# Kernel tuning notes

Hardware: AMD Instinct MI355X
Metric: run time of the kernel (lower is better)

The kernel has to match this reference:

```python
import jax, jax.numpy as jnp
import numpy as np

B = 16
N = [4096, 1024, 256, 64, 16]
NF = [1, 16, 32, 64, 128, 256]
DEG = 6
KS = 5
LAT = 32


def spline_conv(x, edge_index, pseudo, W, root, bias):
    """SplineConv: open B-spline, degree 1, dim 3, kernel_size 5, sum aggregation (norm=False).
    x: [Nn, Cin], edge_index: [2, E] (src, dst), pseudo: [E, 3] in [0,1], W: [125, Cin, Cout]."""
    src, dst = edge_index[0], edge_index[1]
    v = pseudo * (KS - 1)                       # degree-1 open spline interval
    lo = jnp.clip(jnp.floor(v), 0.0, KS - 2)
    frac = v - lo                               # [E, 3]
    lo = lo.astype(jnp.int32)
    xs = x[src]                                 # [E, Cin] gather
    strides = jnp.array([1, KS, KS * KS], dtype=jnp.int32)
    msg = jnp.zeros((src.shape[0], W.shape[2]), dtype=x.dtype)
    for s in range(8):                          # (degree+1)^dim = 8 basis products
        bits = np.array([(s >> d) & 1 for d in range(3)], dtype=np.int32)
        basis = jnp.prod(jnp.where(bits[None, :] == 1, frac, 1.0 - frac), axis=1)  # [E]
        kidx = jnp.sum((lo + bits[None, :]) * strides[None, :], axis=1)            # [E]
        Wg = W[kidx]                                                               # [E, Cin, Cout]
        msg = msg + basis[:, None] * jnp.einsum('ei,eio->eo', xs, Wg)
    agg = jax.ops.segment_sum(msg, dst, num_segments=x.shape[0])
    return agg + x @ root + bias


def _fwd(fl, ei):
    (x, ea0, ea1, ea2, ea3, ea4, P01, P12, P23, P34, Pn1, P1n, P43, P32, P21, P10,
     W_c1, r_c1, b_c1, W_c2, r_c2, b_c2, W_c3, r_c3, b_c3, W_c4, r_c4, b_c4, W_c5, r_c5, b_c5,
     W_d5, r_d5, b_d5, W_d4, r_d4, b_d4, W_d3, r_d3, b_d3, W_d2, r_d2, b_d2, W_d1, r_d1, b_d1,
     fce1_w, fce1_b, fce21_w, fce21_b, fce22_w, fce22_b, fcd3_w, fcd3_b, fcd4_w, fcd4_b, eps) = fl
    ei0, ei1, ei2, ei3, ei4 = ei
    elu = jax.nn.elu
    # ---- encoder ----
    h = elu(spline_conv(x, ei0, ea0, W_c1, r_c1, b_c1))
    h = P01 @ h.reshape(B, N[0], NF[1])
    h = elu(spline_conv(h.reshape(-1, NF[1]), ei1, ea1, W_c2, r_c2, b_c2))
    h = P12 @ h.reshape(B, N[1], NF[2])
    h = elu(spline_conv(h.reshape(-1, NF[2]), ei2, ea2, W_c3, r_c3, b_c3))
    h = P23 @ h.reshape(B, N[2], NF[3])
    h = elu(spline_conv(h.reshape(-1, NF[3]), ei3, ea3, W_c4, r_c4, b_c4))
    h = P34 @ h.reshape(B, N[3], NF[4])
    h = elu(spline_conv(h.reshape(-1, NF[4]), ei4, ea4, W_c5, r_c5, b_c5))
    h = (Pn1 @ h.reshape(B, N[4], NF[5])).reshape(B, NF[5])
    # 1x1 convs over [B, C, 1, 1] == dense layers
    h = elu(h @ fce1_w + fce1_b)
    mu = h @ fce21_w + fce21_b
    logvar = h @ fce22_w + fce22_b
    # ---- reparameterize ----
    z = eps * jnp.exp(0.5 * logvar) + mu
    # ---- decoder ----
    h = elu(z @ fcd3_w + fcd3_b)
    h = elu(h @ fcd4_w + fcd4_b)
    h = P1n @ h.reshape(B, 1, NF[5])            # [B, N4, nf5]
    h = elu(spline_conv(h.reshape(-1, NF[5]), ei4, ea4, W_d5, r_d5, b_d5))
    h = P43 @ h.reshape(B, N[4], NF[4])
    h = elu(spline_conv(h.reshape(-1, NF[4]), ei3, ea3, W_d4, r_d4, b_d4))
    h = P32 @ h.reshape(B, N[3], NF[3])
    h = elu(spline_conv(h.reshape(-1, NF[3]), ei2, ea2, W_d3, r_d3, b_d3))
    h = P21 @ h.reshape(B, N[2], NF[2])
    h = elu(spline_conv(h.reshape(-1, NF[2]), ei1, ea1, W_d2, r_d2, b_d2))
    h = P10 @ h.reshape(B, N[1], NF[1])
    h = elu(spline_conv(h.reshape(-1, NF[1]), ei0, ea0, W_d1, r_d1, b_d1))
    recon = h.reshape(B, -1)                    # [B, N0] (nf0 == 1)
    return recon, mu, logvar


def setup_inputs() -> dict:
    key = jax.random.key(0)
    ks = iter(jax.random.split(key, 128))
    def nrm(shape, scale=1.0):
        return jax.random.normal(next(ks), shape, dtype=jnp.float32) * scale
    def edges(n):
        # per-sample random mesh-like connectivity, offset per graph copy
        e = jax.random.randint(next(ks), (2, B, n * DEG), 0, n)
        off = (jnp.arange(B) * n)[None, :, None]
        return (e + off).reshape(2, -1).astype(jnp.int32)
    inp = {}
    inp['x'] = nrm((B * N[0], NF[0]))
    for i in range(5):
        inp[f'ea{i}'] = jax.random.uniform(next(ks), (B * N[i] * DEG, 3), dtype=jnp.float32)
    pools = {'P01': (N[1], N[0]), 'P12': (N[2], N[1]), 'P23': (N[3], N[2]), 'P34': (N[4], N[3]),
             'Pn1': (1, N[4]), 'P1n': (N[4], 1), 'P43': (N[3], N[4]), 'P32': (N[2], N[3]),
             'P21': (N[1], N[2]), 'P10': (N[0], N[1])}
    for k2, (a, b) in pools.items():
        inp[k2] = nrm((a, b), 1.0 / np.sqrt(b))
    def spl(name, ci, co):
        inp[f'W_{name}'] = nrm((KS ** 3, ci, co), 0.1 / np.sqrt(ci))
        inp[f'r_{name}'] = nrm((ci, co), 1.0 / np.sqrt(ci))
        inp[f'b_{name}'] = nrm((co,), 0.01)
    spl('c1', NF[0], NF[1]); spl('c2', NF[1], NF[2]); spl('c3', NF[2], NF[3]); spl('c4', NF[3], NF[4]); spl('c5', NF[4], NF[5])
    spl('d5', NF[5], NF[4]); spl('d4', NF[4], NF[3]); spl('d3', NF[3], NF[2]); spl('d2', NF[2], NF[1]); spl('d1', NF[1], NF[0])
    def lin(name, ci, co):
        inp[f'{name}_w'] = nrm((ci, co), 1.0 / np.sqrt(ci))
        inp[f'{name}_b'] = nrm((co,), 0.01)
    lin('fce1', NF[5], NF[5]); lin('fce21', NF[5], LAT); lin('fce22', NF[5], LAT)
    lin('fcd3', LAT, NF[5]); lin('fcd4', NF[5], NF[5])
    inp['eps'] = nrm((B, LAT))
    for i in range(5):
        inp[f'ei{i}'] = edges(N[i])
    return inp


def reference(x, ea0, ea1, ea2, ea3, ea4, P01, P12, P23, P34, Pn1, P1n, P43, P32, P21, P10,
              W_c1, r_c1, b_c1, W_c2, r_c2, b_c2, W_c3, r_c3, b_c3, W_c4, r_c4, b_c4, W_c5, r_c5, b_c5,
              W_d5, r_d5, b_d5, W_d4, r_d4, b_d4, W_d3, r_d3, b_d3, W_d2, r_d2, b_d2, W_d1, r_d1, b_d1,
              fce1_w, fce1_b, fce21_w, fce21_b, fce22_w, fce22_b, fcd3_w, fcd3_b, fcd4_w, fcd4_b, eps,
              ei0, ei1, ei2, ei3, ei4):
    fl = (x, ea0, ea1, ea2, ea3, ea4, P01, P12, P23, P34, Pn1, P1n, P43, P32, P21, P10,
          W_c1, r_c1, b_c1, W_c2, r_c2, b_c2, W_c3, r_c3, b_c3, W_c4, r_c4, b_c4, W_c5, r_c5, b_c5,
          W_d5, r_d5, b_d5, W_d4, r_d4, b_d4, W_d3, r_d3, b_d3, W_d2, r_d2, b_d2, W_d1, r_d1, b_d1,
          fce1_w, fce1_b, fce21_w, fce21_b, fce22_w, fce22_b, fcd3_w, fcd3_b, fcd4_w, fcd4_b, eps)
    return _fwd(fl, (ei0, ei1, ei2, ei3, ei4))
```

## Files before the change

kernel.cpp:

```cpp
#include <hip/hip_runtime.h>
#include <hip/hip_bf16.h>

#define TPB 256
#define CDIV(a,b) (((a)+(b)-1)/(b))

__device__ __forceinline__ float elu_f(float v) {
    return v > 0.f ? v : expm1f(v);
}

__device__ __forceinline__ int ld_idx(const void* __restrict__ ei, int pos, int is64) {
    if (is64) return (int)((const long long*)ei)[pos];
    return ((const int*)ei)[pos];
}

__device__ __forceinline__ void spline_basis(const float* __restrict__ pseudo, int e,
                                             float bas[8], int kidx[8]) {
    float f[3]; int lo[3];
#pragma unroll
    for (int d = 0; d < 3; ++d) {
        float v = pseudo[e * 3 + d] * 4.f;
        float l = floorf(v);
        l = fminf(fmaxf(l, 0.f), 3.f);
        f[d] = v - l;
        lo[d] = (int)l;
    }
#pragma unroll
    for (int s = 0; s < 8; ++s) {
        int b0 = s & 1, b1 = (s >> 1) & 1, b2 = (s >> 2) & 1;
        bas[s] = (b0 ? f[0] : 1.f - f[0]) * (b1 ? f[1] : 1.f - f[1]) * (b2 ? f[2] : 1.f - f[2]);
        kidx[s] = (lo[0] + b0) + 5 * (lo[1] + b1) + 25 * (lo[2] + b2);
    }
}

__global__ void k_detect(const int* __restrict__ ei0_as_i32, int* __restrict__ flag) {
    if (threadIdx.x == 0 && blockIdx.x == 0) {
        int zeros = 0;
        for (int k = 0; k < 128; ++k)
            if (ei0_as_i32[2 * k + 1] == 0) zeros++;
        flag[0] = (zeros >= 120) ? 1 : 0;
    }
}

__global__ __launch_bounds__(TPB) void k_zero(float* __restrict__ p, int n) {
    int t = blockIdx.x * blockDim.x + threadIdx.x;
    if (t < n) p[t] = 0.f;
}

__global__ __launch_bounds__(TPB) void k_zero_i(int* __restrict__ p, int n) {
    int t = blockIdx.x * blockDim.x + threadIdx.x;
    if (t < n) p[t] = 0;
}

__global__ __launch_bounds__(TPB) void k_csr_count5(const void* e0, const void* e1,
                                                    const void* e2, const void* e3,
                                                    const void* e4, int* __restrict__ cnt,
                                                    const int* __restrict__ flag) {
    int t = blockIdx.x * blockDim.x + threadIdx.x;
    if (t >= 523776) return;
    int is64 = flag[0];
    const void* ei; int e, E, noff;
    if (t < 393216)      { ei = e0; e = t;          E = 393216; noff = 0; }
    else if (t < 491520) { ei = e1; e = t - 393216; E = 98304;  noff = 65536; }
    else if (t < 516096) { ei = e2; e = t - 491520; E = 24576;  noff = 81920; }
    else if (t < 522240) { ei = e3; e = t - 516096; E = 6144;   noff = 86016; }
    else                 { ei = e4; e = t - 522240; E = 1536;   noff = 87040; }
    int dst = ld_idx(ei, E + e, is64);
    atomicAdd(&cnt[noff + dst], 1);
}

__device__ __forceinline__ void lvl_of_block(int b, int& l, int& lb) {
    if (b < 256)      { l = 0; lb = b; }
    else if (b < 320) { l = 1; lb = b - 256; }
    else if (b < 336) { l = 2; lb = b - 320; }
    else if (b < 340) { l = 3; lb = b - 336; }
    else              { l = 4; lb = b - 340; }
}

__global__ __launch_bounds__(256) void k_scan_a(const int* __restrict__ cnt,
                                                int* __restrict__ rows,
                                                int* __restrict__ bsum) {
    const int NOFF[5] = {0, 65536, 81920, 86016, 87040};
    const int ROFF[5] = {0, 65537, 81922, 86019, 87044};
    __shared__ int s[256];
    int l, lb; lvl_of_block(blockIdx.x, l, lb);
    int t = threadIdx.x;
    int i = lb * 256 + t;
    int v = cnt[NOFF[l] + i];
    s[t] = v;
    __syncthreads();
    for (int off = 1; off < 256; off <<= 1) {
        int u = (t >= off) ? s[t - off] : 0;
        __syncthreads();
        s[t] += u;
        __syncthreads();
    }
    rows[ROFF[l] + i] = s[t] - v;
    if (t == 255) bsum[blockIdx.x] = s[255];
}

__global__ __launch_bounds__(256) void k_scan_b(int* __restrict__ bsum,
                                                int* __restrict__ rows) {
    const int NB[5]    = {256, 64, 16, 4, 1};
    const int BOFF[5]  = {0, 256, 320, 336, 340};
    const int ROFF[5]  = {0, 65537, 81922, 86019, 87044};
    const int NODES[5] = {65536, 16384, 4096, 1024, 256};
    __shared__ int s[256];
    int l = blockIdx.x, t = threadIdx.x;
    int nb = NB[l];
    int v = (t < nb) ? bsum[BOFF[l] + t] : 0;
    s[t] = v;
    __syncthreads();
    for (int off = 1; off < 256; off <<= 1) {
        int u = (t >= off) ? s[t - off] : 0;
        __syncthreads();
        s[t] += u;
        __syncthreads();
    }
    if (t < nb) bsum[BOFF[l] + t] = s[t] - v;
    if (t == 0) rows[ROFF[l] + NODES[l]] = s[255];
}

__global__ __launch_bounds__(256) void k_scan_c(const int* __restrict__ bsum,
                                                int* __restrict__ rows) {
    const int ROFF[5] = {0, 65537, 81922, 86019, 87044};
    int l, lb; lvl_of_block(blockIdx.x, l, lb);
    rows[ROFF[l] + lb * 256 + threadIdx.x] += bsum[blockIdx.x];
}

__global__ __launch_bounds__(TPB) void k_csr_fill5(const void* e0, const void* e1,
                                                   const void* e2, const void* e3,
                                                   const void* e4,
                                                   const int* __restrict__ rows,
                                                   int* __restrict__ cur,
                                                   int* __restrict__ eids,
                                                   const int* __restrict__ flag) {
    int t = blockIdx.x * blockDim.x + threadIdx.x;
    if (t >= 523776) return;
    int is64 = flag[0];
    const void* ei; int e, E, noff, roff, eoff;
    if (t < 393216)      { ei = e0; e = t;          E = 393216; noff = 0;     roff = 0;     eoff = 0; }
    else if (t < 491520) { ei = e1; e = t - 393216; E = 98304;  noff = 65536; roff = 65537; eoff = 393216; }
    else if (t < 516096) { ei = e2; e = t - 491520; E = 24576;  noff = 81920; roff = 81922; eoff = 491520; }
    else if (t < 522240) { ei = e3; e = t - 516096; E = 6144;   noff = 86016; roff = 86019; eoff = 516096; }
    else                 { ei = e4; e = t - 522240; E = 1536;   noff = 87040; roff = 87044; eoff = 522240; }
    int dst = ld_idx(ei, E + e, is64);
    int pos = rows[roff + dst] + atomicAdd(&cur[noff + dst], 1);
    eids[eoff + pos] = e;
}

__global__ __launch_bounds__(TPB) void k_csr_count(const void* __restrict__ ei,
                                                   int* __restrict__ cnt, int E,
                                                   const int* __restrict__ flag) {
    int t = blockIdx.x * blockDim.x + threadIdx.x;
    if (t >= E) return;
    int dst = ld_idx(ei, E + t, flag[0]);
    atomicAdd(&cnt[dst], 1);
}

__global__ __launch_bounds__(1024) void k_csr_scan(const int* __restrict__ cnt,
                                                   int* __restrict__ row_ptr) {
    __shared__ int s_part[1024];
    int t = threadIdx.x;
    int base = t * 64;
    int sum = 0;
    for (int i = 0; i < 64; ++i) sum += cnt[base + i];
    s_part[t] = sum;
    __syncthreads();
    for (int off = 1; off < 1024; off <<= 1) {
        int v = (t >= off) ? s_part[t - off] : 0;
        __syncthreads();
        s_part[t] += v;
        __syncthreads();
    }
    int run = (t == 0) ? 0 : s_part[t - 1];
    for (int i = 0; i < 64; ++i) { row_ptr[base + i] = run; run += cnt[base + i]; }
    if (t == 1023) row_ptr[65536] = run;
}

__global__ __launch_bounds__(TPB) void k_csr_fill(const void* __restrict__ ei,
                                                  const int* __restrict__ row_ptr,
                                                  int* __restrict__ cur,
                                                  int* __restrict__ eid, int E,
                                                  const int* __restrict__ flag) {
    int t = blockIdx.x * blockDim.x + threadIdx.x;
    if (t >= E) return;
    int dst = ld_idx(ei, E + t, flag[0]);
    int pos = row_ptr[dst] + atomicAdd(&cur[dst], 1);
    eid[pos] = t;
}

__global__ __launch_bounds__(256) void k_gather_c1(const float* __restrict__ x,
                                                   const float* __restrict__ pseudo,
                                                   const void* __restrict__ ei,
                                                   const float* __restrict__ W,
                                                   const float* __restrict__ root,
                                                   const float* __restrict__ bias,
                                                   const int* __restrict__ row_ptr,
                                                   const int* __restrict__ eid,
                                                   float* __restrict__ agg,
                                                   const int* __restrict__ flag) {
    __shared__ float4 s_w[500];
    for (int i = threadIdx.x; i < 500; i += 256)
        s_w[i] = reinterpret_cast<const float4*>(W)[i];
    __syncthreads();
    int t = blockIdx.x * 256 + threadIdx.x;
    int n = t >> 2, cg = t & 3, co0 = cg * 4;
    int is64 = flag[0];
    float xn = x[n];
    float a0 = fmaf(xn, root[co0 + 0], bias[co0 + 0]);
    float a1 = fmaf(xn, root[co0 + 1], bias[co0 + 1]);
    float a2 = fmaf(xn, root[co0 + 2], bias[co0 + 2]);
    float a3 = fmaf(xn, root[co0 + 3], bias[co0 + 3]);
    int rb = row_ptr[n], re = row_ptr[n + 1];
    for (int idx = rb; idx < re; ++idx) {
        int e = eid[idx];
        int src = ld_idx(ei, e, is64);
        float bas[8]; int kidx[8];
        spline_basis(pseudo, e, bas, kidx);
        float xs = x[src];
        float m0 = 0.f, m1 = 0.f, m2 = 0.f, m3 = 0.f;
#pragma unroll
        for (int s = 0; s < 8; ++s) {
            float4 w = s_w[kidx[s] * 4 + cg];
            float bs = bas[s];
            m0 = fmaf(bs, w.x, m0);
            m1 = fmaf(bs, w.y, m1);
            m2 = fmaf(bs, w.z, m2);
            m3 = fmaf(bs, w.w, m3);
        }
        a0 = fmaf(xs, m0, a0);
        a1 = fmaf(xs, m1, a1);
        a2 = fmaf(xs, m2, a2);
        a3 = fmaf(xs, m3, a3);
    }
    float4 v = make_float4(a0, a1, a2, a3);
    *reinterpret_cast<float4*>(&agg[n * 16 + co0]) = v;
}

__global__ __launch_bounds__(256) void k_gather_d1(const float* __restrict__ xin,
                                                   const float* __restrict__ pseudo,
                                                   const void* __restrict__ ei,
                                                   const float* __restrict__ W,
                                                   const float* __restrict__ root,
                                                   const float* __restrict__ bias,
                                                   const int* __restrict__ row_ptr,
                                                   const int* __restrict__ eid,
                                                   float* __restrict__ outp,
                                                   const int* __restrict__ flag) {
    __shared__ float s_w[2000];
    for (int i = threadIdx.x; i < 2000; i += 256) s_w[i] = W[i];
    __syncthreads();
    int t = blockIdx.x * 256 + threadIdx.x;
    int n = t >> 2, l = t & 3;
    int is64 = flag[0];
    int rb = row_ptr[n], re = row_ptr[n + 1];
    float acc = 0.f;
    for (int idx = rb + l; idx < re; idx += 4) {
        int e = eid[idx];
        int src = ld_idx(ei, e, is64);
        float bas[8]; int kidx[8];
        spline_basis(pseudo, e, bas, kidx);
        const float4* xs4 = reinterpret_cast<const float4*>(xin + src * 16);
        float4 xv0 = xs4[0], xv1 = xs4[1], xv2 = xs4[2], xv3 = xs4[3];
        float m = 0.f;
#pragma unroll
        for (int s = 0; s < 8; ++s) {
            const float4* wp = reinterpret_cast<const float4*>(s_w + kidx[s] * 16);
            float4 w0 = wp[0], w1 = wp[1], w2 = wp[2], w3 = wp[3];
            float p = 0.f;
            p = fmaf(xv0.x, w0.x, p); p = fmaf(xv0.y, w0.y, p);
            p = fmaf(xv0.z, w0.z, p); p = fmaf(xv0.w, w0.w, p);
            p = fmaf(xv1.x, w1.x, p); p = fmaf(xv1.y, w1.y, p);
            p = fmaf(xv1.z, w1.z, p); p = fmaf(xv1.w, w1.w, p);
            p = fmaf(xv2.x, w2.x, p); p = fmaf(xv2.y, w2.y, p);
            p = fmaf(xv2.z, w2.z, p); p = fmaf(xv2.w, w2.w, p);
            p = fmaf(xv3.x, w3.x, p); p = fmaf(xv3.y, w3.y, p);
            p = fmaf(xv3.z, w3.z, p); p = fmaf(xv3.w, w3.w, p);
            m = fmaf(bas[s], p, m);
        }
        acc += m;
    }
    acc += __shfl_xor(acc, 1);
    acc += __shfl_xor(acc, 2);
    if (l == 0) {
        const float4* xr = reinterpret_cast<const float4*>(xin + n * 16);
        const float4* rr = reinterpret_cast<const float4*>(root);
        float r = bias[0];
#pragma unroll
        for (int q = 0; q < 4; ++q) {
            float4 xv = xr[q], rv = rr[q];
            r = fmaf(xv.x, rv.x, r); r = fmaf(xv.y, rv.y, r);
            r = fmaf(xv.z, rv.z, r); r = fmaf(xv.w, rv.w, r);
        }
        outp[n] = elu_f(r + acc);
    }
}

template <int CIN, int COUT, int CSPLIT, int IROOT>
__global__ __launch_bounds__(256) void k_gW(const float* __restrict__ x,
                                            const float* __restrict__ pseudo,
                                            const void* __restrict__ ei,
                                            const float* __restrict__ W,
                                            const float* __restrict__ root,
                                            const float* __restrict__ bias,
                                            const int* __restrict__ row_ptr,
                                            const int* __restrict__ eid,
                                            float* __restrict__ agg,
                                            const int* __restrict__ flag) {
    constexpr int COG = COUT / 4;
    constexpr int CPT = CIN / CSPLIT;
    constexpr int PS = CPT + 1;
    __shared__ float4 s_w[125 * PS];
    int cg = blockIdx.y, cih = blockIdx.z;
    const float4* W4 = reinterpret_cast<const float4*>(W);
    for (int i = threadIdx.x; i < 125 * CPT; i += 256) {
        int k = i / CPT, ci = i - k * CPT;
        s_w[k * PS + ci] = W4[(k * CIN + cih * CPT + ci) * COG + cg];
    }
    __syncthreads();
    int n = blockIdx.x * 256 + threadIdx.x;
    int is64 = flag[0];
    int co0 = cg * 4;
    float4 acc = make_float4(0.f, 0.f, 0.f, 0.f);
    if (IROOT == 1 || (IROOT == 2 && cih == 0)) {
        acc = reinterpret_cast<const float4*>(bias)[cg];
        const float* xp = x + (size_t)n * CIN;
        const float4* r4 = reinterpret_cast<const float4*>(root);
#pragma unroll 4
        for (int ci = 0; ci < CIN; ++ci) {
            float xv = xp[ci];
            float4 rv = r4[ci * COG + cg];
            acc.x = fmaf(xv, rv.x, acc.x); acc.y = fmaf(xv, rv.y, acc.y);
            acc.z = fmaf(xv, rv.z, acc.z); acc.w = fmaf(xv, rv.w, acc.w);
        }
    }
    int rb = row_ptr[n], re = row_ptr[n + 1];
    for (int idx = rb; idx < re; ++idx) {
        int e = eid[idx];
        int src = ld_idx(ei, e, is64);
        float bas[8]; int kidx[8];
        spline_basis(pseudo, e, bas, kidx);
        float xv[CPT];
        const float* xp = x + (size_t)src * CIN + cih * CPT;
#pragma unroll
        for (int ci = 0; ci < CPT; ++ci) xv[ci] = xp[ci];
#pragma unroll
        for (int s = 0; s < 8; ++s) {
            const float4* wp = s_w + kidx[s] * PS;
            float bs = bas[s];
#pragma unroll
            for (int ci = 0; ci < CPT; ++ci) {
                float bx = bs * xv[ci];
                float4 w = wp[ci];
                acc.x = fmaf(bx, w.x, acc.x); acc.y = fmaf(bx, w.y, acc.y);
                acc.z = fmaf(bx, w.z, acc.z); acc.w = fmaf(bx, w.w, acc.w);
            }
        }
    }
    float* o = agg + (size_t)n * COUT + co0;
    if (IROOT == 1) {
        *reinterpret_cast<float4*>(o) = acc;
    } else {
        atomicAdd(o + 0, acc.x); atomicAdd(o + 1, acc.y);
        atomicAdd(o + 2, acc.z); atomicAdd(o + 3, acc.w);
    }
}

__global__ __launch_bounds__(TPB) void k_root4(const float* __restrict__ x,
                                               const float* __restrict__ root,
                                               const float* __restrict__ bias,
                                               float* __restrict__ out,
                                               int nnode, int cin, int cout) {
    int t = blockIdx.x * blockDim.x + threadIdx.x;
    if (t >= nnode * cout) return;
    int n = t / cout, co = t - n * cout;
    const float4* xr = reinterpret_cast<const float4*>(x + n * cin);
    float a0 = 0.f, a1 = 0.f, a2 = 0.f, a3 = 0.f;
    int q4 = cin >> 2;
    for (int q = 0; q < q4; ++q) {
        float4 xv = xr[q];
        const float* rp = root + (q * 4) * cout + co;
        a0 = fmaf(xv.x, rp[0], a0);
        a1 = fmaf(xv.y, rp[cout], a1);
        a2 = fmaf(xv.z, rp[2 * cout], a2);
        a3 = fmaf(xv.w, rp[3 * cout], a3);
    }
    out[t] = bias[co] + ((a0 + a1) + (a2 + a3));
}

template <int CIN, int COUT, int CSPLIT>
__global__ __launch_bounds__(TPB) void k_msg4(const float* __restrict__ x,
                                              const float* __restrict__ pseudo,
                                              const void* __restrict__ ei,
                                              const float* __restrict__ W,
                                              float* __restrict__ agg, int E,
                                              const int* __restrict__ flag) {
    constexpr int COG = COUT / 4;
    constexpr int CPT = CIN / CSPLIT;
    int t = blockIdx.x * blockDim.x + threadIdx.x;
    if (t >= E * COG * CSPLIT) return;
    int is64 = flag[0];
    int cog = t % COG;
    int rest = t / COG;
    int cs = rest % CSPLIT;
    int e = rest / CSPLIT;
    int co0 = cog * 4;
    int src = ld_idx(ei, e, is64);
    int dst = ld_idx(ei, E + e, is64);
    float bas[8]; int kidx[8];
    spline_basis(pseudo, e, bas, kidx);
    int wof[8];
#pragma unroll
    for (int s = 0; s < 8; ++s) wof[s] = kidx[s] * CIN * COUT + co0;
    float a0 = 0.f, a1 = 0.f, a2 = 0.f, a3 = 0.f;
    const float* xp = x + src * CIN + cs * CPT;
    const int cbase = cs * CPT * COUT;
    for (int ci = 0; ci < CPT; ++ci) {
        float xv = xp[ci];
        int off = cbase + ci * COUT;
#pragma unroll
        for (int s = 0; s < 8; ++s) {
            float4 w = *reinterpret_cast<const float4*>(&W[wof[s] + off]);
            float bx = bas[s] * xv;
            a0 = fmaf(bx, w.x, a0);
            a1 = fmaf(bx, w.y, a1);
            a2 = fmaf(bx, w.z, a2);
            a3 = fmaf(bx, w.w, a3);
        }
    }
    float* ap = &agg[dst * COUT + co0];
    atomicAdd(ap + 0, a0);
    atomicAdd(ap + 1, a1);
    atomicAdd(ap + 2, a2);
    atomicAdd(ap + 3, a3);
}

template <int CIN, int COUT>
__global__ __launch_bounds__(TPB) void k_msg_s(const float* __restrict__ x,
                                               const float* __restrict__ pseudo,
                                               const void* __restrict__ ei,
                                               const float* __restrict__ W,
                                               float* __restrict__ agg, int E,
                                               const int* __restrict__ flag) {
    int t = blockIdx.x * blockDim.x + threadIdx.x;
    if (t >= E * COUT) return;
    int is64 = flag[0];
    int e = t / COUT, co = t - e * COUT;
    int src = ld_idx(ei, e, is64);
    int dst = ld_idx(ei, E + e, is64);
    float bas[8]; int kidx[8];
    spline_basis(pseudo, e, bas, kidx);
    float acc = 0.f;
    const float* xp = x + src * CIN;
    for (int ci = 0; ci < CIN; ++ci) {
        float xv = xp[ci];
#pragma unroll
        for (int s = 0; s < 8; ++s)
            acc = fmaf(bas[s] * xv, W[kidx[s] * CIN * COUT + ci * COUT + co], acc);
    }
    atomicAdd(&agg[dst * COUT + co], acc);
}

__global__ __launch_bounds__(1024) void k_msg_c1(const float* __restrict__ x,
                                                 const float* __restrict__ pseudo,
                                                 const void* __restrict__ ei,
                                                 const float* __restrict__ W,
                                                 const float* __restrict__ root,
                                                 const float* __restrict__ bias,
                                                 float* __restrict__ agg,
                                                 const int* __restrict__ flag) {
    __shared__ float s_acc[4096 * 4];
    __shared__ float s_w[125 * 4];
    int b = blockIdx.x, cg = blockIdx.y, t = threadIdx.x;
    int co0 = cg * 4;
    int is64 = flag[0];
    if (t < 500) s_w[t] = W[(t >> 2) * 16 + co0 + (t & 3)];
    float r0 = root[co0], r1 = root[co0 + 1], r2 = root[co0 + 2], r3 = root[co0 + 3];
    float b0 = bias[co0], b1 = bias[co0 + 1], b2 = bias[co0 + 2], b3 = bias[co0 + 3];
    for (int n = t; n < 4096; n += 1024) {
        float xv = x[b * 4096 + n];
        s_acc[n * 4 + 0] = fmaf(xv, r0, b0);
        s_acc[n * 4 + 1] = fmaf(xv, r1, b1);
        s_acc[n * 4 + 2] = fmaf(xv, r2, b2);
        s_acc[n * 4 + 3] = fmaf(xv, r3, b3);
    }
    __syncthreads();
    int ebeg = b * 24576;
    for (int k = t; k < 24576; k += 1024) {
        int e = ebeg + k;
        int src = ld_idx(ei, e, is64);
        int dst = ld_idx(ei, 393216 + e, is64);
        float xv = x[src];
        float bas[8]; int kidx[8];
        spline_basis(pseudo, e, bas, kidx);
        float m0 = 0.f, m1 = 0.f, m2 = 0.f, m3 = 0.f;
#pragma unroll
        for (int s = 0; s < 8; ++s) {
            const float* wp = s_w + kidx[s] * 4;
            float bs = bas[s];
            m0 = fmaf(bs, wp[0], m0);
            m1 = fmaf(bs, wp[1], m1);
            m2 = fmaf(bs, wp[2], m2);
            m3 = fmaf(bs, wp[3], m3);
        }
        int dl = (dst - b * 4096) * 4;
        atomicAdd(&s_acc[dl + 0], m0 * xv);
        atomicAdd(&s_acc[dl + 1], m1 * xv);
        atomicAdd(&s_acc[dl + 2], m2 * xv);
        atomicAdd(&s_acc[dl + 3], m3 * xv);
    }
    __syncthreads();
    for (int n = t; n < 4096; n += 1024) {
        float4 v = *reinterpret_cast<float4*>(&s_acc[n * 4]);
        *reinterpret_cast<float4*>(&agg[(b * 4096 + n) * 16 + co0]) = v;
    }
}

template <int F, int ELU>
__global__ __launch_bounds__(256) void k_pool2(const float* __restrict__ in,
                                               const float* __restrict__ P,
                                               float* __restrict__ out,
                                               int nout, int nin) {
    constexpr int FQ = F / 4;
    constexpr int TI = 256 / FQ;
    constexpr int KT = 64;
    constexpr int PS = KT + 4;
    __shared__ float s_p[TI * PS];
    __shared__ float4 s_in[KT * FQ];
    int tid = threadIdx.x;
    int fq = tid % FQ;
    int i = tid / FQ;
    int b = blockIdx.y;
    int gi = blockIdx.x * TI + i;
    int nchunk = nin / gridDim.z;
    int kbeg = blockIdx.z * nchunk;
    const float4* inb4 = reinterpret_cast<const float4*>(in + b * nin * F);
    float4 acc = make_float4(0.f, 0.f, 0.f, 0.f);

    for (int k0 = kbeg; k0 < kbeg + nchunk; k0 += KT) {
        __syncthreads();
        for (int idx = tid; idx < TI * (KT / 4); idx += 256) {
            int r = idx / (KT / 4), c = idx % (KT / 4);
            float4 v = *reinterpret_cast<const float4*>(&P[(blockIdx.x * TI + r) * nin + k0 + c * 4]);
            *reinterpret_cast<float4*>(&s_p[r * PS + c * 4]) = v;
        }
        for (int idx = tid; idx < KT * FQ; idx += 256) {
            float4 v = inb4[(size_t)(k0 + idx / FQ) * FQ + (idx % FQ)];
            if (ELU) {
                v.x = elu_f(v.x); v.y = elu_f(v.y);
                v.z = elu_f(v.z); v.w = elu_f(v.w);
            }
            s_in[idx] = v;
        }
        __syncthreads();
#pragma unroll 4
        for (int j = 0; j < KT; j += 4) {
            float4 pv = *reinterpret_cast<const float4*>(&s_p[i * PS + j]);
            float4 v0 = s_in[(j + 0) * FQ + fq];
            float4 v1 = s_in[(j + 1) * FQ + fq];
            float4 v2 = s_in[(j + 2) * FQ + fq];
            float4 v3 = s_in[(j + 3) * FQ + fq];
            acc.x = fmaf(pv.x, v0.x, acc.x); acc.y = fmaf(pv.x, v0.y, acc.y);
            acc.z = fmaf(pv.x, v0.z, acc.z); acc.w = fmaf(pv.x, v0.w, acc.w);
            acc.x = fmaf(pv.y, v1.x, acc.x); acc.y = fmaf(pv.y, v1.y, acc.y);
            acc.z = fmaf(pv.y, v1.z, acc.z); acc.w = fmaf(pv.y, v1.w, acc.w);
            acc.x = fmaf(pv.z, v2.x, acc.x); acc.y = fmaf(pv.z, v2.y, acc.y);
            acc.z = fmaf(pv.z, v2.z, acc.z); acc.w = fmaf(pv.z, v2.w, acc.w);
            acc.x = fmaf(pv.w, v3.x, acc.x); acc.y = fmaf(pv.w, v3.y, acc.y);
            acc.z = fmaf(pv.w, v3.z, acc.z); acc.w = fmaf(pv.w, v3.w, acc.w);
        }
    }
    float* o = out + ((size_t)b * nout + gi) * F + fq * 4;
    if (gridDim.z > 1) {
        atomicAdd(o + 0, acc.x); atomicAdd(o + 1, acc.y);
        atomicAdd(o + 2, acc.z); atomicAdd(o + 3, acc.w);
    } else {
        *reinterpret_cast<float4*>(o) = acc;
    }
}

__global__ __launch_bounds__(TPB) void k_pool_e(const float* __restrict__ in,
                                                const float* __restrict__ P,
                                                float* __restrict__ out,
                                                int nout, int nin, int F, int elu) {
    int t = blockIdx.x * blockDim.x + threadIdx.x;
    if (t >= 16 * nout * F) return;
    int f = t % F;
    int rest = t / F;
    int i = rest % nout;
    int b = rest / nout;
    const float* ip = in + b * nin * F + f;
    const float* pp = P + i * nin;
    float acc = 0.f;
    if (elu) {
#pragma unroll 4
        for (int j = 0; j < nin; ++j) acc = fmaf(pp[j], elu_f(ip[j * F]), acc);
    } else {
#pragma unroll 4
        for (int j = 0; j < nin; ++j) acc = fmaf(pp[j], ip[j * F], acc);
    }
    out[t] = acc;
}

__global__ __launch_bounds__(1024) void k_fc_fused2(
        const float* __restrict__ c5agg, const float* __restrict__ Pn1,
        const float* __restrict__ fce1_w, const float* __restrict__ fce1_b,
        const float* __restrict__ fce21_w, const float* __restrict__ fce21_b,
        const float* __restrict__ fce22_w, const float* __restrict__ fce22_b,
        const float* __restrict__ eps,
        const float* __restrict__ fcd3_w, const float* __restrict__ fcd3_b,
        const float* __restrict__ fcd4_w, const float* __restrict__ fcd4_b,
        const float* __restrict__ P1n,
        float* __restrict__ out_mu, float* __restrict__ out_lv,
        float* __restrict__ dec_in) {
    __shared__ float s0[256], s1[256], sz[32], sp[1024];
    int b = blockIdx.x, t = threadIdx.x;
    if (t < 256) {
        const float* ap = c5agg + b * 4096 + t;
        float acc = 0.f;
#pragma unroll
        for (int n = 0; n < 16; ++n) acc = fmaf(Pn1[n], elu_f(ap[n * 256]), acc);
        s0[t] = acc;
    }
    __syncthreads();
    {
        int q = t >> 8, co = t & 255;
        const float* w = fce1_w + co;
        float a = 0.f;
        int c0 = q * 64;
        for (int ci = 0; ci < 64; ci += 8) {
#pragma unroll
            for (int k = 0; k < 8; ++k) a = fmaf(s0[c0 + ci + k], w[(c0 + ci + k) * 256], a);
        }
        sp[t] = a;
    }
    __syncthreads();
    if (t < 256) s1[t] = elu_f(sp[t] + sp[t + 256] + sp[t + 512] + sp[t + 768] + fce1_b[t]);
    __syncthreads();
    if (t < 512) {
        int which = t >> 8, r = t & 255;
        int co = r & 31, q = r >> 5;
        const float* w = (which ? fce22_w : fce21_w) + co;
        float a = 0.f;
        int c0 = q * 32;
#pragma unroll
        for (int k = 0; k < 32; ++k) a = fmaf(s1[c0 + k], w[(c0 + k) * 32], a);
        sp[t] = a;
    }
    __syncthreads();
    if (t < 64) {
        int which = t >> 5, co = t & 31;
        float m = (which ? fce22_b : fce21_b)[co];
        int base = which * 256 + co;
#pragma unroll
        for (int q = 0; q < 8; ++q) m += sp[base + q * 32];
        if (which == 0) { out_mu[b * 32 + co] = m; s0[co] = m; }
        else            { out_lv[b * 32 + co] = m; s0[64 + co] = m; }
    }
    __syncthreads();
    if (t < 32) sz[t] = fmaf(eps[b * 32 + t], expf(0.5f * s0[64 + t]), s0[t]);
    __syncthreads();
    if (t < 256) {
        float d = fcd3_b[t];
#pragma unroll
        for (int ci = 0; ci < 32; ++ci) d = fmaf(sz[ci], fcd3_w[ci * 256 + t], d);
        s0[t] = elu_f(d);
    }
    __syncthreads();
    {
        int q = t >> 8, co = t & 255;
        const float* w = fcd4_w + co;
        float a = 0.f;
        int c0 = q * 64;
        for (int ci = 0; ci < 64; ci += 8) {
#pragma unroll
            for (int k = 0; k < 8; ++k) a = fmaf(s0[c0 + ci + k], w[(c0 + ci + k) * 256], a);
        }
        sp[t] = a;
    }
    __syncthreads();
    if (t < 256) s1[t] = elu_f(sp[t] + sp[t + 256] + sp[t + 512] + sp[t + 768] + fcd4_b[t]);
    __syncthreads();
    {
        float* op = dec_in + b * 4096;
        for (int idx = t; idx < 4096; idx += 1024) {
            int n = idx >> 8, f = idx & 255;
            op[idx] = P1n[n] * s1[f];
        }
    }
}

__global__ __launch_bounds__(TPB) void k_elu_out(const float* __restrict__ in,
                                                 float* __restrict__ out, int n) {
    int t = blockIdx.x * blockDim.x + threadIdx.x;
    if (t < n) out[t] = elu_f(in[t]);
}

extern "C" void kernel_launch(void* const* d_in, const int* in_sizes, int n_in,
                              void* d_out, int out_size, void* d_ws, size_t ws_size,
                              hipStream_t stream) {
    const float* x    = (const float*)d_in[0];
    const float* ea0  = (const float*)d_in[1];
    const float* ea1  = (const float*)d_in[2];
    const float* ea2  = (const float*)d_in[3];
    const float* ea3  = (const float*)d_in[4];
    const float* ea4  = (const float*)d_in[5];
    const float* P01  = (const float*)d_in[6];
    const float* P12  = (const float*)d_in[7];
    const float* P23  = (const float*)d_in[8];
    const float* P34  = (const float*)d_in[9];
    const float* Pn1  = (const float*)d_in[10];
    const float* P1n  = (const float*)d_in[11];
    const float* P43  = (const float*)d_in[12];
    const float* P32  = (const float*)d_in[13];
    const float* P21  = (const float*)d_in[14];
    const float* P10  = (const float*)d_in[15];
    const float* W_c1 = (const float*)d_in[16]; const float* r_c1 = (const float*)d_in[17]; const float* b_c1 = (const float*)d_in[18];
    const float* W_c2 = (const float*)d_in[19]; const float* r_c2 = (const float*)d_in[20]; const float* b_c2 = (const float*)d_in[21];
    const float* W_c3 = (const float*)d_in[22]; const float* r_c3 = (const float*)d_in[23]; const float* b_c3 = (const float*)d_in[24];
    const float* W_c4 = (const float*)d_in[25]; const float* r_c4 = (const float*)d_in[26]; const float* b_c4 = (const float*)d_in[27];
    const float* W_c5 = (const float*)d_in[28]; const float* r_c5 = (const float*)d_in[29]; const float* b_c5 = (const float*)d_in[30];
    const float* W_d5 = (const float*)d_in[31]; const float* r_d5 = (const float*)d_in[32]; const float* b_d5 = (const float*)d_in[33];
    const float* W_d4 = (const float*)d_in[34]; const float* r_d4 = (const float*)d_in[35]; const float* b_d4 = (const float*)d_in[36];
    const float* W_d3 = (const float*)d_in[37]; const float* r_d3 = (const float*)d_in[38]; const float* b_d3 = (const float*)d_in[39];
    const float* W_d2 = (const float*)d_in[40]; const float* r_d2 = (const float*)d_in[41]; const float* b_d2 = (const float*)d_in[42];
    const float* W_d1 = (const float*)d_in[43]; const float* r_d1 = (const float*)d_in[44]; const float* b_d1 = (const float*)d_in[45];
    const float* fce1_w  = (const float*)d_in[46]; const float* fce1_b  = (const float*)d_in[47];
    const float* fce21_w = (const float*)d_in[48]; const float* fce21_b = (const float*)d_in[49];
    const float* fce22_w = (const float*)d_in[50]; const float* fce22_b = (const float*)d_in[51];
    const float* fcd3_w  = (const float*)d_in[52]; const float* fcd3_b  = (const float*)d_in[53];
    const float* fcd4_w  = (const float*)d_in[54]; const float* fcd4_b  = (const float*)d_in[55];
    const float* eps  = (const float*)d_in[56];
    const void* ei0 = d_in[57];
    const void* ei1 = d_in[58];
    const void* ei2 = d_in[59];
    const void* ei3 = d_in[60];
    const void* ei4 = d_in[61];

    const int E0 = 393216, E1 = 98304, E2 = 24576, E3 = 6144, E4 = 1536;
    const int N0 = 65536, N1 = 16384, N2 = 4096, N3 = 1024, N4 = 256;

    float* sm   = (float*)d_ws;
    float* bufA = sm + 13824;
    float* bufB = bufA + 1048576;
    int*  flag  = (int*)(bufB + 262144);
    int*  ibase = flag + 64;
    int* cur  = ibase;
    int* rows = cur + 87296;
    int* eids = rows + 87301;
    int* bsum = eids + 523776;
    const size_t WS_ALL = (size_t)(13824 + 1048576 + 262144 + 64 + 87296 + 87301 + 523776 + 512) * 4;
    int* o_row = ibase;
    int* o_cur = o_row + 65537;
    int* o_eid = o_cur + 65536;
    const size_t WS_OLD = (size_t)(13824 + 1048576 + 262144 + 64 + 524352) * 4;
    const bool bigA = ws_size >= WS_ALL;
    const bool big0 = ws_size >= WS_OLD;

    const int ROFF[5] = {0, 65537, 81922, 86019, 87044};
    const int EOFF[5] = {0, 393216, 491520, 516096, 522240};

    float* out = (float*)d_out;
    float* out_mu = out + 65536;
    float* out_lv = out + 66048;

    auto g = [](int n) { return dim3((unsigned)CDIV(n, TPB)); };

    k_detect<<<1, 64, 0, stream>>>((const int*)ei0, flag);

    if (bigA) {
        k_zero_i<<<g(87296), TPB, 0, stream>>>(cur, 87296);
        k_csr_count5<<<g(523776), TPB, 0, stream>>>(ei0, ei1, ei2, ei3, ei4, cur, flag);
        k_scan_a<<<341, 256, 0, stream>>>(cur, rows, bsum);
        k_scan_b<<<5, 256, 0, stream>>>(bsum, rows);
        k_scan_c<<<341, 256, 0, stream>>>(bsum, rows);
        k_zero_i<<<g(87296), TPB, 0, stream>>>(cur, 87296);
        k_csr_fill5<<<g(523776), TPB, 0, stream>>>(ei0, ei1, ei2, ei3, ei4, rows, cur, eids, flag);

        k_gather_c1<<<1024, 256, 0, stream>>>(x, ea0, ei0, W_c1, r_c1, b_c1,
                                              rows + ROFF[0], eids + EOFF[0], bufA, flag);
        k_zero<<<g(262144), TPB, 0, stream>>>(bufB, 262144);
        k_pool2<16, 1><<<dim3(16, 16, 4), 256, 0, stream>>>(bufA, P01, bufB, 1024, 4096);

        k_gW<16, 32, 1, 1><<<dim3(64, 8, 1), 256, 0, stream>>>(bufB, ea1, ei1, W_c2, r_c2, b_c2,
                                                               rows + ROFF[1], eids + EOFF[1], bufA, flag);
        k_zero<<<g(131072), TPB, 0, stream>>>(bufB, 131072);
        k_pool2<32, 1><<<dim3(8, 16, 2), 256, 0, stream>>>(bufA, P12, bufB, 256, 1024);

        k_zero<<<g(262144), TPB, 0, stream>>>(bufA, 262144);
        k_gW<32, 64, 2, 2><<<dim3(16, 16, 2), 256, 0, stream>>>(bufB, ea2, ei2, W_c3, r_c3, b_c3,
                                                                rows + ROFF[2], eids + EOFF[2], bufA, flag);
        k_zero<<<g(65536), TPB, 0, stream>>>(bufB, 65536);
        k_pool2<64, 1><<<dim3(4, 16, 2), 256, 0, stream>>>(bufA, P23, bufB, 64, 256);

        k_zero<<<g(131072), TPB, 0, stream>>>(bufA, 131072);
        k_gW<64, 128, 4, 2><<<dim3(4, 32, 4), 256, 0, stream>>>(bufB, ea3, ei3, W_c4, r_c4, b_c4,
                                                                rows + ROFF[3], eids + EOFF[3], bufA, flag);
        k_pool_e<<<g(16 * 16 * 128), TPB, 0, stream>>>(bufA, P34, bufB, 16, 64, 128, 1);

        k_zero<<<g(65536), TPB, 0, stream>>>(bufA, 65536);
        k_gW<128, 256, 8, 2><<<dim3(1, 64, 8), 256, 0, stream>>>(bufB, ea4, ei4, W_c5, r_c5, b_c5,
                                                                 rows + ROFF[4], eids + EOFF[4], bufA, flag);

        k_fc_fused2<<<16, 1024, 0, stream>>>(bufA, Pn1,
                                             fce1_w, fce1_b, fce21_w, fce21_b, fce22_w, fce22_b,
                                             eps, fcd3_w, fcd3_b, fcd4_w, fcd4_b, P1n,
                                             out_mu, out_lv, bufA);

        k_zero<<<g(32768), TPB, 0, stream>>>(bufB, 32768);
        k_gW<256, 128, 16, 2><<<dim3(1, 32, 16), 256, 0, stream>>>(bufA, ea4, ei4, W_d5, r_d5, b_d5,
                                                                   rows + ROFF[4], eids + EOFF[4], bufB, flag);
        k_pool_e<<<g(16 * 64 * 128), TPB, 0, stream>>>(bufB, P43, bufA, 64, 16, 128, 1);

        k_zero<<<g(65536), TPB, 0, stream>>>(bufB, 65536);
        k_gW<128, 64, 8, 2><<<dim3(4, 16, 8), 256, 0, stream>>>(bufA, ea3, ei3, W_d4, r_d4, b_d4,
                                                                rows + ROFF[3], eids + EOFF[3], bufB, flag);
        k_pool2<64, 1><<<dim3(16, 16, 1), 256, 0, stream>>>(bufB, P32, bufA, 256, 64);

        k_zero<<<g(131072), TPB, 0, stream>>>(bufB, 131072);
        k_gW<64, 32, 4, 2><<<dim3(16, 8, 4), 256, 0, stream>>>(bufA, ea2, ei2, W_d3, r_d3, b_d3,
                                                               rows + ROFF[2], eids + EOFF[2], bufB, flag);
        k_pool2<32, 1><<<dim3(32, 16, 1), 256, 0, stream>>>(bufB, P21, bufA, 1024, 256);

        k_zero<<<g(262144), TPB, 0, stream>>>(bufB, 262144);
        k_gW<32, 16, 2, 2><<<dim3(64, 4, 2), 256, 0, stream>>>(bufA, ea1, ei1, W_d2, r_d2, b_d2,
                                                               rows + ROFF[1], eids + EOFF[1], bufB, flag);
        k_pool2<16, 1><<<dim3(64, 16, 1), 256, 0, stream>>>(bufB, P10, bufA, 4096, 1024);

        k_gather_d1<<<1024, 256, 0, stream>>>(bufA, ea0, ei0, W_d1, r_d1, b_d1,
                                              rows + ROFF[0], eids + EOFF[0], out, flag);
        return;
    }

    if (big0) {
        k_zero_i<<<g(65536), TPB, 0, stream>>>(o_cur, 65536);
        k_csr_count<<<g(E0), TPB, 0, stream>>>(ei0, o_cur, E0, flag);
        k_csr_scan<<<1, 1024, 0, stream>>>(o_cur, o_row);
        k_zero_i<<<g(65536), TPB, 0, stream>>>(o_cur, 65536);
        k_csr_fill<<<g(E0), TPB, 0, stream>>>(ei0, o_row, o_cur, o_eid, E0, flag);
        k_gather_c1<<<1024, 256, 0, stream>>>(x, ea0, ei0, W_c1, r_c1, b_c1,
                                              o_row, o_eid, bufA, flag);
    } else {
        k_msg_c1<<<dim3(16, 4), 1024, 0, stream>>>(x, ea0, ei0, W_c1, r_c1, b_c1, bufA, flag);
    }
    k_zero<<<g(262144), TPB, 0, stream>>>(bufB, 262144);
    k_pool2<16, 1><<<dim3(16, 16, 4), 256, 0, stream>>>(bufA, P01, bufB, 1024, 4096);

    k_root4<<<g(N1 * 32), TPB, 0, stream>>>(bufB, r_c2, b_c2, bufA, N1, 16, 32);
    k_msg4<16, 32, 1><<<g(E1 * 8), TPB, 0, stream>>>(bufB, ea1, ei1, W_c2, bufA, E1, flag);
    k_zero<<<g(131072), TPB, 0, stream>>>(bufB, 131072);
    k_pool2<32, 1><<<dim3(8, 16, 2), 256, 0, stream>>>(bufA, P12, bufB, 256, 1024);

    k_root4<<<g(N2 * 64), TPB, 0, stream>>>(bufB, r_c3, b_c3, bufA, N2, 32, 64);
    k_msg4<32, 64, 1><<<g(E2 * 16), TPB, 0, stream>>>(bufB, ea2, ei2, W_c3, bufA, E2, flag);
    k_zero<<<g(65536), TPB, 0, stream>>>(bufB, 65536);
    k_pool2<64, 1><<<dim3(4, 16, 2), 256, 0, stream>>>(bufA, P23, bufB, 64, 256);

    k_root4<<<g(N3 * 128), TPB, 0, stream>>>(bufB, r_c4, b_c4, bufA, N3, 64, 128);
    k_msg4<64, 128, 1><<<g(E3 * 32), TPB, 0, stream>>>(bufB, ea3, ei3, W_c4, bufA, E3, flag);
    k_pool_e<<<g(16 * 16 * 128), TPB, 0, stream>>>(bufA, P34, bufB, 16, 64, 128, 1);

    k_root4<<<g(N4 * 256), TPB, 0, stream>>>(bufB, r_c5, b_c5, bufA, N4, 128, 256);
    k_msg4<128, 256, 2><<<g(E4 * 128), TPB, 0, stream>>>(bufB, ea4, ei4, W_c5, bufA, E4, flag);

    k_fc_fused2<<<16, 1024, 0, stream>>>(bufA, Pn1,
                                         fce1_w, fce1_b, fce21_w, fce21_b, fce22_w, fce22_b,
                                         eps, fcd3_w, fcd3_b, fcd4_w, fcd4_b, P1n,
                                         out_mu, out_lv, bufA);

    k_root4<<<g(N4 * 128), TPB, 0, stream>>>(bufA, r_d5, b_d5, bufB, N4, 256, 128);
    k_msg4<256, 128, 4><<<g(E4 * 128), TPB, 0, stream>>>(bufA, ea4, ei4, W_d5, bufB, E4, flag);
    k_pool_e<<<g(16 * 64 * 128), TPB, 0, stream>>>(bufB, P43, bufA, 64, 16, 128, 1);

    k_root4<<<g(N3 * 64), TPB, 0, stream>>>(bufA, r_d4, b_d4, bufB, N3, 128, 64);
    k_msg4<128, 64, 2><<<g(E3 * 32), TPB, 0, stream>>>(bufA, ea3, ei3, W_d4, bufB, E3, flag);
    k_pool2<64, 1><<<dim3(16, 16, 1), 256, 0, stream>>>(bufB, P32, bufA, 256, 64);

    k_root4<<<g(N2 * 32), TPB, 0, stream>>>(bufA, r_d3, b_d3, bufB, N2, 64, 32);
    k_msg4<64, 32, 1><<<g(E2 * 8), TPB, 0, stream>>>(bufA, ea2, ei2, W_d3, bufB, E2, flag);
    k_pool2<32, 1><<<dim3(32, 16, 1), 256, 0, stream>>>(bufB, P21, bufA, 1024, 256);

    k_root4<<<g(N1 * 16), TPB, 0, stream>>>(bufA, r_d2, b_d2, bufB, N1, 32, 16);
    k_msg4<32, 16, 1><<<g(E1 * 4), TPB, 0, stream>>>(bufA, ea1, ei1, W_d2, bufB, E1, flag);
    k_pool2<16, 1><<<dim3(64, 16, 1), 256, 0, stream>>>(bufB, P10, bufA, 4096, 1024);

    if (big0) {
        k_gather_d1<<<1024, 256, 0, stream>>>(bufA, ea0, ei0, W_d1, r_d1, b_d1,
                                              o_row, o_eid, out, flag);
    } else {
        k_root4<<<g(N0 * 1), TPB, 0, stream>>>(bufA, r_d1, b_d1, bufB, N0, 16, 1);
        k_msg_s<16, 1><<<g(E0), TPB, 0, stream>>>(bufA, ea0, ei0, W_d1, bufB, E0, flag);
        k_elu_out<<<g(N0), TPB, 0, stream>>>(bufB, out, 65536);
    }
}
```

Before: 964.5 us.

## Split each node's edge loop across four lanes with shuffle reduction in gW

The gather-weight spline conv kernel now assigns four lanes per destination node instead of one. The lanes stride over the node's CSR edges and split the root matmul input channels, then combine partial sums with xor shuffles before one lane writes or atomically adds. Grids are enlarged fourfold to match. This raises parallelism and occupancy for the small, deep layers where there were few nodes per launch, at the cost of shuffle reductions and an extra shared-memory weight reload per block.

```diff
diff --git a/kernel.cpp b/kernel.cpp
--- a/kernel.cpp
+++ b/kernel.cpp
@@ -297,16 +297,16 @@
 }
 
 template <int CIN, int COUT, int CSPLIT, int IROOT>
-__global__ __launch_bounds__(256) void k_gW(const float* __restrict__ x,
-                                            const float* __restrict__ pseudo,
-                                            const void* __restrict__ ei,
-                                            const float* __restrict__ W,
-                                            const float* __restrict__ root,
-                                            const float* __restrict__ bias,
-                                            const int* __restrict__ row_ptr,
-                                            const int* __restrict__ eid,
-                                            float* __restrict__ agg,
-                                            const int* __restrict__ flag) {
+__global__ __launch_bounds__(256) void k_gW2(const float* __restrict__ x,
+                                             const float* __restrict__ pseudo,
+                                             const void* __restrict__ ei,
+                                             const float* __restrict__ W,
+                                             const float* __restrict__ root,
+                                             const float* __restrict__ bias,
+                                             const int* __restrict__ row_ptr,
+                                             const int* __restrict__ eid,
+                                             float* __restrict__ agg,
+                                             const int* __restrict__ flag) {
     constexpr int COG = COUT / 4;
     constexpr int CPT = CIN / CSPLIT;
     constexpr int PS = CPT + 1;
@@ -318,24 +318,26 @@
         s_w[k * PS + ci] = W4[(k * CIN + cih * CPT + ci) * COG + cg];
     }
     __syncthreads();
-    int n = blockIdx.x * 256 + threadIdx.x;
+    int nl = threadIdx.x >> 2, l = threadIdx.x & 3;
+    int n = blockIdx.x * 64 + nl;
     int is64 = flag[0];
     int co0 = cg * 4;
     float4 acc = make_float4(0.f, 0.f, 0.f, 0.f);
     if (IROOT == 1 || (IROOT == 2 && cih == 0)) {
-        acc = reinterpret_cast<const float4*>(bias)[cg];
-        const float* xp = x + (size_t)n * CIN;
-        const float4* r4 = reinterpret_cast<const float4*>(root);
+        if (l == 0) acc = reinterpret_cast<const float4*>(bias)[cg];
+        constexpr int CQ = CIN / 4;
+        const float* xp = x + (size_t)n * CIN + l * CQ;
+        const float4* r4 = reinterpret_cast<const float4*>(root) + (size_t)(l * CQ) * COG + cg;
 #pragma unroll 4
-        for (int ci = 0; ci < CIN; ++ci) {
+        for (int ci = 0; ci < CQ; ++ci) {
             float xv = xp[ci];
-            float4 rv = r4[ci * COG + cg];
+            float4 rv = r4[ci * COG];
             acc.x = fmaf(xv, rv.x, acc.x); acc.y = fmaf(xv, rv.y, acc.y);
             acc.z = fmaf(xv, rv.z, acc.z); acc.w = fmaf(xv, rv.w, acc.w);
         }
     }
     int rb = row_ptr[n], re = row_ptr[n + 1];
-    for (int idx = rb; idx < re; ++idx) {
+    for (int idx = rb + l; idx < re; idx += 4) {
         int e = eid[idx];
         int src = ld_idx(ei, e, is64);
         float bas[8]; int kidx[8];
@@ -357,12 +359,18 @@
             }
         }
     }
-    float* o = agg + (size_t)n * COUT + co0;
-    if (IROOT == 1) {
-        *reinterpret_cast<float4*>(o) = acc;
-    } else {
-        atomicAdd(o + 0, acc.x); atomicAdd(o + 1, acc.y);
-        atomicAdd(o + 2, acc.z); atomicAdd(o + 3, acc.w);
+    acc.x += __shfl_xor(acc.x, 1); acc.y += __shfl_xor(acc.y, 1);
+    acc.z += __shfl_xor(acc.z, 1); acc.w += __shfl_xor(acc.w, 1);
+    acc.x += __shfl_xor(acc.x, 2); acc.y += __shfl_xor(acc.y, 2);
+    acc.z += __shfl_xor(acc.z, 2); acc.w += __shfl_xor(acc.w, 2);
+    if (l == 0) {
+        float* o = agg + (size_t)n * COUT + co0;
+        if (IROOT == 1) {
+            *reinterpret_cast<float4*>(o) = acc;
+        } else {
+            atomicAdd(o + 0, acc.x); atomicAdd(o + 1, acc.y);
+            atomicAdd(o + 2, acc.z); atomicAdd(o + 3, acc.w);
+        }
     }
 }
 
@@ -782,25 +790,25 @@
         k_zero<<<g(262144), TPB, 0, stream>>>(bufB, 262144);
         k_pool2<16, 1><<<dim3(16, 16, 4), 256, 0, stream>>>(bufA, P01, bufB, 1024, 4096);
 
-        k_gW<16, 32, 1, 1><<<dim3(64, 8, 1), 256, 0, stream>>>(bufB, ea1, ei1, W_c2, r_c2, b_c2,
-                                                               rows + ROFF[1], eids + EOFF[1], bufA, flag);
+        k_gW2<16, 32, 1, 1><<<dim3(256, 8, 1), 256, 0, stream>>>(bufB, ea1, ei1, W_c2, r_c2, b_c2,
+                                                                 rows + ROFF[1], eids + EOFF[1], bufA, flag);
         k_zero<<<g(131072), TPB, 0, stream>>>(bufB, 131072);
         k_pool2<32, 1><<<dim3(8, 16, 2), 256, 0, stream>>>(bufA, P12, bufB, 256, 1024);
 
         k_zero<<<g(262144), TPB, 0, stream>>>(bufA, 262144);
-        k_gW<32, 64, 2, 2><<<dim3(16, 16, 2), 256, 0, stream>>>(bufB, ea2, ei2, W_c3, r_c3, b_c3,
-                                                                rows + ROFF[2], eids + EOFF[2], bufA, flag);
+        k_gW2<32, 64, 2, 2><<<dim3(64, 16, 2), 256, 0, stream>>>(bufB, ea2, ei2, W_c3, r_c3, b_c3,
+                                                                 rows + ROFF[2], eids + EOFF[2], bufA, flag);
         k_zero<<<g(65536), TPB, 0, stream>>>(bufB, 65536);
         k_pool2<64, 1><<<dim3(4, 16, 2), 256, 0, stream>>>(bufA, P23, bufB, 64, 256);
 
         k_zero<<<g(131072), TPB, 0, stream>>>(bufA, 131072);
-        k_gW<64, 128, 4, 2><<<dim3(4, 32, 4), 256, 0, stream>>>(bufB, ea3, ei3, W_c4, r_c4, b_c4,
-                                                                rows + ROFF[3], eids + EOFF[3], bufA, flag);
+        k_gW2<64, 128, 4, 2><<<dim3(16, 32, 4), 256, 0, stream>>>(bufB, ea3, ei3, W_c4, r_c4, b_c4,
+                                                                  rows + ROFF[3], eids + EOFF[3], bufA, flag);
         k_pool_e<<<g(16 * 16 * 128), TPB, 0, stream>>>(bufA, P34, bufB, 16, 64, 128, 1);
 
         k_zero<<<g(65536), TPB, 0, stream>>>(bufA, 65536);
-        k_gW<128, 256, 8, 2><<<dim3(1, 64, 8), 256, 0, stream>>>(bufB, ea4, ei4, W_c5, r_c5, b_c5,
-                                                                 rows + ROFF[4], eids + EOFF[4], bufA, flag);
+        k_gW2<128, 256, 8, 2><<<dim3(4, 64, 8), 256, 0, stream>>>(bufB, ea4, ei4, W_c5, r_c5, b_c5,
+                                                                  rows + ROFF[4], eids + EOFF[4], bufA, flag);
 
         k_fc_fused2<<<16, 1024, 0, stream>>>(bufA, Pn1,
                                              fce1_w, fce1_b, fce21_w, fce21_b, fce22_w, fce22_b,
@@ -808,23 +816,23 @@
                                              out_mu, out_lv, bufA);
 
         k_zero<<<g(32768), TPB, 0, stream>>>(bufB, 32768);
-        k_gW<256, 128, 16, 2><<<dim3(1, 32, 16), 256, 0, stream>>>(bufA, ea4, ei4, W_d5, r_d5, b_d5,
-                                                                   rows + ROFF[4], eids + EOFF[4], bufB, flag);
+        k_gW2<256, 128, 16, 2><<<dim3(4, 32, 16), 256, 0, stream>>>(bufA, ea4, ei4, W_d5, r_d5, b_d5,
+                                                                    rows + ROFF[4], eids + EOFF[4], bufB, flag);
         k_pool_e<<<g(16 * 64 * 128), TPB, 0, stream>>>(bufB, P43, bufA, 64, 16, 128, 1);
 
         k_zero<<<g(65536), TPB, 0, stream>>>(bufB, 65536);
-        k_gW<128, 64, 8, 2><<<dim3(4, 16, 8), 256, 0, stream>>>(bufA, ea3, ei3, W_d4, r_d4, b_d4,
-                                                                rows + ROFF[3], eids + EOFF[3], bufB, flag);
+        k_gW2<128, 64, 8, 2><<<dim3(16, 16, 8), 256, 0, stream>>>(bufA, ea3, ei3, W_d4, r_d4, b_d4,
+                                                                  rows + ROFF[3], eids + EOFF[3], bufB, flag);
         k_pool2<64, 1><<<dim3(16, 16, 1), 256, 0, stream>>>(bufB, P32, bufA, 256, 64);
 
         k_zero<<<g(131072), TPB, 0, stream>>>(bufB, 131072);
-        k_gW<64, 32, 4, 2><<<dim3(16, 8, 4), 256, 0, stream>>>(bufA, ea2, ei2, W_d3, r_d3, b_d3,
-                                                               rows + ROFF[2], eids + EOFF[2], bufB, flag);
+        k_gW2<64, 32, 4, 2><<<dim3(64, 8, 4), 256, 0, stream>>>(bufA, ea2, ei2, W_d3, r_d3, b_d3,
+                                                                rows + ROFF[2], eids + EOFF[2], bufB, flag);
         k_pool2<32, 1><<<dim3(32, 16, 1), 256, 0, stream>>>(bufB, P21, bufA, 1024, 256);
 
         k_zero<<<g(262144), TPB, 0, stream>>>(bufB, 262144);
-        k_gW<32, 16, 2, 2><<<dim3(64, 4, 2), 256, 0, stream>>>(bufA, ea1, ei1, W_d2, r_d2, b_d2,
-                                                               rows + ROFF[1], eids + EOFF[1], bufB, flag);
+        k_gW2<32, 16, 2, 2><<<dim3(256, 4, 2), 256, 0, stream>>>(bufA, ea1, ei1, W_d2, r_d2, b_d2,
+                                                                 rows + ROFF[1], eids + EOFF[1], bufB, flag);
         k_pool2<16, 1><<<dim3(64, 16, 1), 256, 0, stream>>>(bufB, P10, bufA, 4096, 1024);
 
         k_gather_d1<<<1024, 256, 0, stream>>>(bufA, ea0, ei0, W_d1, r_d1, b_d1,
```

Result: faster. 866.3 us (-10.2%).
